# Optimization experiments

Hardware: AMD Instinct MI355X
Metric: run time of the kernel (lower is better)

## Reference

```python
import jax, jax.numpy as jnp
import numpy as np

TOPK = 80
RADIUS_GAIN = 14.0
RADIUS_MIN = 1.5
RADIUS_MAX = 18.0
EPS = 1e-6


def _norm01(x, eps=EPS):
    # per-batch min/max normalization over all non-batch dims
    b = x.shape[0]
    flat = x.reshape(b, -1)
    mn = flat.min(axis=1).reshape(b, 1, 1, 1)
    mx = flat.max(axis=1).reshape(b, 1, 1, 1)
    return (x - mn) / (mx - mn + eps)


def _avg_pool(x, k):
    # torch avg_pool2d(kernel=k, stride=1, padding=k//2, count_include_pad=True)
    s = jax.lax.reduce_window(x, 0.0, jax.lax.add, (1, 1, k, k), (1, 1, 1, 1), 'SAME')
    return s / float(k * k)


def _max_pool(x, k):
    return jax.lax.reduce_window(x, -jnp.inf, jax.lax.max, (1, 1, k, k), (1, 1, 1, 1), 'SAME')


def _compact_connected_prior(score_map):
    occ = (score_map > 0.2).astype(score_map.dtype)
    local_occ = _avg_pool(occ, 9)
    local_mass = _avg_pool(score_map, 9)
    compact = _norm01(local_occ * local_mass)
    return score_map * compact


def _gaussian_map(score_map, depth):
    b, _, h, w = score_map.shape
    dtype = score_map.dtype
    pooled = _max_pool(score_map, 5)
    maxima = score_map * (score_map == pooled).astype(dtype)  # NMS keep local maxima

    flat = maxima.reshape(b, h * w)
    vals, inds = jax.lax.top_k(flat, TOPK)              # [B,K]
    vals = jnp.where(vals > 0, vals, jnp.zeros_like(vals))  # zero-weight masked peaks

    ys = (inds // w).astype(dtype)                       # [B,K]
    xs = (inds % w).astype(dtype)
    z = jnp.take_along_axis(depth.reshape(b, h * w), inds, axis=1)
    z = jnp.maximum(z, 1e-3)
    radius = jnp.clip(RADIUS_GAIN / z, RADIUS_MIN, RADIUS_MAX)
    sigma2 = (0.6 * radius) ** 2                         # [B,K]

    yy = jnp.arange(h, dtype=dtype)
    xx = jnp.arange(w, dtype=dtype)
    dx2 = (xx[None, None, None, :] - xs[:, :, None, None]) ** 2   # [B,K,1,W]
    dy2 = (yy[None, None, :, None] - ys[:, :, None, None]) ** 2   # [B,K,H,1]
    maps = vals[:, :, None, None] * jnp.exp(
        -(dx2 + dy2) / (2.0 * sigma2[:, :, None, None] + 1e-6))    # [B,K,H,W]
    gauss = maps.max(axis=1)[:, None]                    # [B,1,H,W]; maps>=0 so zero baseline preserved
    return _norm01(gauss)


def setup_inputs() -> dict:
    key = jax.random.key(0)
    k1, k2 = jax.random.split(key)
    B, H, W = 8, 320, 320
    voxel_score_map = jax.random.uniform(k1, (B, 1, H, W), dtype=jnp.float32)
    # depth within the module's valid z range [0.3, 20.0]
    depth = 0.3 + 19.7 * jax.random.uniform(k2, (B, 1, H, W), dtype=jnp.float32)
    return {'voxel_score_map': voxel_score_map, 'depth': depth}


def reference(voxel_score_map, depth):
    compact_score = _compact_connected_prior(voxel_score_map)
    return _gaussian_map(compact_score, depth)
```

## Files before the change

kernel.cpp:

```cpp
#include <hip/hip_runtime.h>
#include <math.h>

#define HH 320
#define WW 320
#define HWP (HH * WW)
#define KTOP 80
#define CNT_STRIDE 64
#define CAP (HWP / 2)
#define TS 16
#define TPR (WW / TS)
#define TPI (TPR * (HH / TS))
#define TW 32
#define TH 64
#define NTPRX (WW / TW)
#define NTPI (NTPRX * (HH / TH))
#define LOG2E 1.4426950408889634f
#define NLOG2TAU 19.931568569324174f

__device__ __forceinline__ void wave_minmax(float& mn, float& mx) {
    for (int off = 32; off > 0; off >>= 1) {
        mn = fminf(mn, __shfl_xor(mn, off, 64));
        mx = fmaxf(mx, __shfl_xor(mx, off, 64));
    }
}

__global__ void pool_fused_k(const float* __restrict__ score, float* __restrict__ prod,
                             float2* __restrict__ pmm, int* __restrict__ cand_cnt, int B_) {
    int tid = threadIdx.x;
    if (blockIdx.x == 0)
        for (int t = tid; t < B_ * CNT_STRIDE; t += 256) cand_cnt[t] = 0;
    int blk = blockIdx.x;
    int b = blk / NTPI, t = blk % NTPI;
    int ty0 = (t / NTPRX) * TH, tx0 = (t % NTPRX) * TW;
    __shared__ float rss[TH + 8][TW + 4];
    __shared__ float rso[TH + 8][TW + 4];
    const float4* img4 = (const float4*)(score + b * HWP);
    for (int i = tid; i < (TH + 8) * (TW / 4); i += 256) {
        int r = i / (TW / 4), q = i % (TW / 4);
        int gy = ty0 - 4 + r;
        float o0=0,o1=0,o2=0,o3=0,p0=0,p1=0,p2=0,p3=0;
        if (gy >= 0 && gy < HH) {
            const float4* row4 = img4 + gy * (WW / 4);
            int gq = tx0 / 4 + q;
            float4 a = (gq > 0) ? row4[gq - 1] : make_float4(0,0,0,0);
            float4 bb = row4[gq];
            float4 c = (gq < WW / 4 - 1) ? row4[gq + 1] : make_float4(0,0,0,0);
            float w0=a.x,w1=a.y,w2=a.z,w3=a.w,w4=bb.x,w5=bb.y,w6=bb.z,w7=bb.w,w8=c.x,w9=c.y,w10=c.z,w11=c.w;
            float s = w0+w1+w2+w3+w4+w5+w6+w7+w8;
            o0=s; s+=w9-w0; o1=s; s+=w10-w1; o2=s; s+=w11-w2; o3=s;
            float c0=(w0>0.2f)?1.f:0.f, c1=(w1>0.2f)?1.f:0.f, c2=(w2>0.2f)?1.f:0.f, c3=(w3>0.2f)?1.f:0.f;
            float c4=(w4>0.2f)?1.f:0.f, c5=(w5>0.2f)?1.f:0.f, c6=(w6>0.2f)?1.f:0.f, c7=(w7>0.2f)?1.f:0.f;
            float c8=(w8>0.2f)?1.f:0.f, c9=(w9>0.2f)?1.f:0.f, c10=(w10>0.2f)?1.f:0.f, c11=(w11>0.2f)?1.f:0.f;
            float u = c0+c1+c2+c3+c4+c5+c6+c7+c8;
            p0=u; u+=c9-c0; p1=u; u+=c10-c1; p2=u; u+=c11-c2; p3=u;
        }
        *(float4*)&rss[r][q * 4] = make_float4(o0,o1,o2,o3);
        *(float4*)&rso[r][q * 4] = make_float4(p0,p1,p2,p3);
    }
    __syncthreads();
    float tmn = INFINITY, tmx = 0.f;
    const float inv81 = 1.0f / 81.0f;
    float4* pr4 = (float4*)(prod + b * HWP);
    for (int i = tid; i < TH * (TW / 4); i += 256) {
        int r = i / (TW / 4), q = i % (TW / 4);
        float sx=0,sy=0,sz=0,sw=0, ox=0,oy=0,oz=0,ow=0;
#pragma unroll
        for (int j = 0; j < 9; ++j) {
            float4 s = *(float4*)&rss[r + j][q * 4];
            float4 o = *(float4*)&rso[r + j][q * 4];
            sx+=s.x; sy+=s.y; sz+=s.z; sw+=s.w;
            ox+=o.x; oy+=o.y; oz+=o.z; ow+=o.w;
        }
        float px=(ox*inv81)*(sx*inv81), py=(oy*inv81)*(sy*inv81);
        float pz=(oz*inv81)*(sz*inv81), pw=(ow*inv81)*(sw*inv81);
        pr4[(ty0 + r) * (WW / 4) + tx0 / 4 + q] = make_float4(px,py,pz,pw);
        tmn = fminf(tmn, fminf(fminf(px,py), fminf(pz,pw)));
        tmx = fmaxf(tmx, fmaxf(fmaxf(px,py), fmaxf(pz,pw)));
    }
    wave_minmax(tmn, tmx);
    __shared__ float wmn[4], wmx[4];
    int w = tid >> 6;
    if ((tid & 63) == 0) { wmn[w] = tmn; wmx[w] = tmx; }
    __syncthreads();
    if (tid == 0)
        pmm[blk] = make_float2(fminf(fminf(wmn[0],wmn[1]), fminf(wmn[2],wmn[3])),
                               fmaxf(fmaxf(wmx[0],wmx[1]), fmaxf(wmx[2],wmx[3])));
}

__global__ void cs_nms_k(const float* __restrict__ score, const float* __restrict__ prod,
                         const float2* __restrict__ pmm, float* __restrict__ cand_base,
                         int* __restrict__ cand_cnt) {
    int tid = threadIdx.x;
    int blk = blockIdx.x;
    int b = blk / NTPI, t = blk % NTPI;
    int ty0 = (t / NTPRX) * TH, tx0 = (t % NTPRX) * TW;
    float tmn = INFINITY, tmx = 0.f;
    if (tid < NTPI) { float2 e = pmm[b * NTPI + tid]; tmn = e.x; tmx = e.y; }
    wave_minmax(tmn, tmx);
    __shared__ float s_mn, s_inv;
    if (tid == 0) { s_mn = tmn; s_inv = 1.0f / (tmx - tmn + 1e-6f); }
    __shared__ float cs[TH + 4][TW + 8 + 4];
    __shared__ float rm[TH + 4][TW + 4];
    __syncthreads();
    float mn = s_mn, inv = s_inv;
    const float4* sc4 = (const float4*)(score + b * HWP);
    const float4* pr4 = (const float4*)(prod + b * HWP);
    for (int i = tid; i < (TH + 4) * 10; i += 256) {
        int r = i / 10, q = i % 10;
        int gy = ty0 - 2 + r;
        int gq = tx0 / 4 - 1 + q;
        float4 c4 = make_float4(0,0,0,0);
        if (gy >= 0 && gy < HH && gq >= 0 && gq < WW / 4) {
            float4 s4 = sc4[gy * (WW / 4) + gq];
            float4 p4 = pr4[gy * (WW / 4) + gq];
            c4.x = s4.x * ((p4.x - mn) * inv); c4.y = s4.y * ((p4.y - mn) * inv);
            c4.z = s4.z * ((p4.z - mn) * inv); c4.w = s4.w * ((p4.w - mn) * inv);
        }
        *(float4*)&cs[r][q * 4] = c4;
    }
    __syncthreads();
    for (int i = tid; i < (TH + 4) * (TW / 4); i += 256) {
        int r = i / (TW / 4), x = (i % (TW / 4)) * 4;
        float c0=cs[r][x+2], c1=cs[r][x+3], c2=cs[r][x+4], c3=cs[r][x+5];
        float c4v=cs[r][x+6], c5=cs[r][x+7], c6=cs[r][x+8], c7=cs[r][x+9];
        float m01=fmaxf(c0,c1), m23=fmaxf(c2,c3), m45=fmaxf(c4v,c5), m67=fmaxf(c6,c7);
        float r0 = fmaxf(fmaxf(m01, m23), c4v);
        float r1 = fmaxf(fmaxf(c1, m23), m45);
        float r2 = fmaxf(fmaxf(m23, m45), c6);
        float r3 = fmaxf(fmaxf(c3, m45), m67);
        *(float4*)&rm[r][x] = make_float4(r0,r1,r2,r3);
    }
    __syncthreads();
    bool cd[8]; float vv[8]; int pb[2]; int offs[8];
#pragma unroll
    for (int qq = 0; qq < 2; ++qq) {
        int quad = qq * 256 + tid;
        int r = quad >> 3, x = (quad & 7) * 4;
        float4 v = *(float4*)&cs[r + 2][x + 4];
        float4 nm = *(float4*)&rm[r][x];
#pragma unroll
        for (int k = 1; k <= 4; ++k) {
            float4 rr = *(float4*)&rm[r + k][x];
            nm.x=fmaxf(nm.x,rr.x); nm.y=fmaxf(nm.y,rr.y);
            nm.z=fmaxf(nm.z,rr.z); nm.w=fmaxf(nm.w,rr.w);
        }
        pb[qq] = (ty0 + r) * WW + tx0 + x;
        cd[qq*4+0] = v.x > 0.f && v.x >= nm.x; vv[qq*4+0] = v.x;
        cd[qq*4+1] = v.y > 0.f && v.y >= nm.y; vv[qq*4+1] = v.y;
        cd[qq*4+2] = v.z > 0.f && v.z >= nm.z; vv[qq*4+2] = v.z;
        cd[qq*4+3] = v.w > 0.f && v.w >= nm.w; vv[qq*4+3] = v.w;
    }
    int lane = tid & 63, w = tid >> 6;
    unsigned long long lower = (1ULL << lane) - 1ULL;
    int wave_run = 0;
#pragma unroll
    for (int j = 0; j < 8; ++j) {
        unsigned long long m = __ballot(cd[j]);
        offs[j] = wave_run + __popcll(m & lower);
        wave_run += __popcll(m);
    }
    __shared__ int wbase[4];
    __shared__ int blockbase;
    if (lane == 0) wbase[w] = wave_run;
    __syncthreads();
    if (tid == 0) {
        int a0=wbase[0], a1=wbase[1], a2=wbase[2], a3=wbase[3];
        int tot = a0+a1+a2+a3;
        wbase[0]=0; wbase[1]=a0; wbase[2]=a0+a1; wbase[3]=a0+a1+a2;
        blockbase = tot ? atomicAdd(&cand_cnt[b * CNT_STRIDE], tot) : 0;
    }
    __syncthreads();
    float* cv = cand_base + b * HWP;
    int* ci = (int*)(cand_base + b * HWP + CAP);
    int bb2 = blockbase + wbase[w];
#pragma unroll
    for (int j = 0; j < 8; ++j) {
        if (cd[j]) {
            int slot = bb2 + offs[j];
            if (slot < CAP) { cv[slot] = vv[j]; ci[slot] = pb[j >> 2] + (j & 3); }
        }
    }
}

__global__ void topk_k(const float* __restrict__ cand_base, const int* __restrict__ cand_cnt,
                       const float* __restrict__ depth, float4* __restrict__ pk4g) {
    int b = blockIdx.x;
    int tid = threadIdx.x;
    int n = cand_cnt[b * CNT_STRIDE];
    if (n > CAP) n = CAP;
    const float* cv = cand_base + b * HWP;
    const int* ci = (const int*)(cand_base + b * HWP + CAP);

    __shared__ int hist[256];
    __shared__ unsigned s_prefix;
    __shared__ int s_kth;
    __shared__ float sel_v[KTOP];
    __shared__ int sel_i[KTOP];
    __shared__ int s_ng, s_nt;
    __shared__ int tie_i[512];

    if (tid == 0) { s_prefix = 0; s_kth = KTOP; s_ng = 0; s_nt = 0; }
    if (tid < KTOP) { sel_v[tid] = 0.f; sel_i[tid] = -1; }
    __syncthreads();

    if (n > KTOP) {
        for (int shift = 24; shift >= 0; shift -= 8) {
            if (tid < 256) hist[tid] = 0;
            __syncthreads();
            unsigned pref = s_prefix;
            unsigned hmask = (shift == 24) ? 0u : (0xFFFFFFFFu << (shift + 8));
            for (int i = tid; i < n; i += 1024) {
                unsigned u = __float_as_uint(cv[i]);
                if ((u & hmask) == (pref & hmask))
                    atomicAdd(&hist[(u >> shift) & 255], 1);
            }
            __syncthreads();
            if (tid < 64) {
                int h0 = hist[tid*4+0], h1 = hist[tid*4+1], h2 = hist[tid*4+2], h3 = hist[tid*4+3];
                int ls3 = h3, ls2 = h2 + ls3, ls1 = h1 + ls2, ls0 = h0 + ls1;
                int sum = ls0;
                for (int off = 1; off < 64; off <<= 1) {
                    int vv2 = __shfl_down(sum, off, 64);
                    if (tid + off < 64) sum += vv2;
                }
                int excl = sum - ls0;
                int kth = s_kth;
                int SS0=ls0+excl, SS1=ls1+excl, SS2=ls2+excl, SS3=ls3+excl, SS4=excl;
                unsigned pr = s_prefix;
                int bin = -1, rem = 0;
                if (SS0 >= kth && SS1 < kth) { bin = tid*4+0; rem = kth - SS1; }
                else if (SS1 >= kth && SS2 < kth) { bin = tid*4+1; rem = kth - SS2; }
                else if (SS2 >= kth && SS3 < kth) { bin = tid*4+2; rem = kth - SS3; }
                else if (SS3 >= kth && SS4 < kth) { bin = tid*4+3; rem = kth - SS4; }
                if (bin >= 0) { s_prefix = pr | ((unsigned)bin << shift); s_kth = rem; }
            }
            __syncthreads();
        }
        unsigned T = s_prefix;
        int need_eq = s_kth;
        for (int i = tid; i < n; i += 1024) {
            unsigned u = __float_as_uint(cv[i]);
            if (u > T) {
                int s2 = atomicAdd(&s_ng, 1);
                if (s2 < KTOP) { sel_v[s2] = cv[i]; sel_i[s2] = ci[i]; }
            } else if (u == T) {
                int s2 = atomicAdd(&s_nt, 1);
                if (s2 < 512) tie_i[s2] = ci[i];
            }
        }
        __syncthreads();
        int G = s_ng; if (G > KTOP) G = KTOP;
        int nt = s_nt; if (nt > 512) nt = 512;
        for (int t = tid; t < nt; t += 1024) {
            int mine = tie_i[t];
            int rank = 0;
            for (int j = 0; j < nt; ++j)
                if (tie_i[j] < mine) rank++;
            if (rank < need_eq && G + rank < KTOP) {
                sel_v[G + rank] = __uint_as_float(T);
                sel_i[G + rank] = mine;
            }
        }
        __syncthreads();
    } else {
        for (int i = tid; i < n; i += 1024) { sel_v[i] = cv[i]; sel_i[i] = ci[i]; }
        __syncthreads();
    }

    if (tid < KTOP) {
        float val = sel_v[tid];
        int idx = sel_i[tid];
        float xk = 0.f, yk = 0.f, wv = -1.f, lv = -INFINITY;
        if (val > 0.f && idx >= 0) {
            yk = (float)(idx / WW);
            xk = (float)(idx % WW);
            float z = fmaxf(depth[b * HWP + idx], 1e-3f);
            float r = fminf(fmaxf(14.0f / z, 1.5f), 18.0f);
            float s2 = 0.6f * r;
            s2 = s2 * s2;
            wv = -LOG2E / (2.0f * s2 + 1e-6f);
            lv = log2f(val);
        }
        pk4g[b * KTOP + tid] = make_float4(lv, xk, yk, wv);
    }
}

__global__ void gauss_tiled_k(const float4* __restrict__ pk4g, float* __restrict__ gauss,
                              float2* __restrict__ gmm) {
    int tb = blockIdx.x, tid = threadIdx.x;
    int b = tb / TPI, t = tb % TPI;
    int ty = t / TPR, tx = t % TPR;
    __shared__ float4 spk[KTOP];
    __shared__ int s_c0, s_cnt;
    bool keep = false;
    float4 pk;
    if (tid < KTOP) {
        pk = pk4g[b * KTOP + tid];
        float cut = (pk.x + NLOG2TAU) / (-pk.w);
        float x0 = (float)(tx * TS), x1 = x0 + (TS - 1);
        float y0 = (float)(ty * TS), y1 = y0 + (TS - 1);
        float cx = fminf(fmaxf(pk.y, x0), x1);
        float cy = fminf(fmaxf(pk.z, y0), y1);
        float dx = pk.y - cx, dy = pk.z - cy;
        keep = (dx * dx + dy * dy) <= cut;
    }
    int lane = tid & 63, w = tid >> 6;
    unsigned long long m = __ballot(keep);
    if (w == 0 && lane == 0) s_c0 = __popcll(m);
    __syncthreads();
    int base = (w == 0) ? 0 : s_c0;
    if (keep) spk[base + __popcll(m & ((1ULL << lane) - 1ULL))] = pk;
    if (w == 1 && lane == 0) s_cnt = s_c0 + __popcll(m);
    __syncthreads();
    int cnt = s_cnt;
    int ly = tid / TS, lx = tid % TS;
    int y = ty * TS + ly, x = tx * TS + lx;
    float fx = (float)x, fy = (float)y;
    float mval = 0.f;
    for (int i = 0; i < cnt; ++i) {
        float4 p = spk[i];
        float dx = fx - p.y, dy = fy - p.z;
        mval = fmaxf(mval, __builtin_amdgcn_exp2f(fmaf(fmaf(dx, dx, dy * dy), p.w, p.x)));
    }
    gauss[b * HWP + y * WW + x] = mval;
    float tmn = mval, tmx = mval;
    wave_minmax(tmn, tmx);
    __shared__ float wmn[4], wmx[4];
    if (lane == 0) { wmn[w] = tmn; wmx[w] = tmx; }
    __syncthreads();
    if (tid == 0)
        gmm[tb] = make_float2(fminf(fminf(wmn[0],wmn[1]), fminf(wmn[2],wmn[3])),
                              fmaxf(fmaxf(wmx[0],wmx[1]), fmaxf(wmx[2],wmx[3])));
}

__global__ void norm_k(const float* __restrict__ gauss, const float2* __restrict__ gmm,
                       float* __restrict__ out, int total) {
    int g4 = blockIdx.x * 256 + threadIdx.x;
    int b = (blockIdx.x * 1024) / HWP;
    float tmn = INFINITY, tmx = 0.f;
    {
        int t = threadIdx.x;
        if (t < TPI) { float2 e = gmm[b * TPI + t]; tmn = e.x; tmx = e.y; }
        int t2 = t + 256;
        if (t2 < TPI) { float2 e = gmm[b * TPI + t2]; tmn = fminf(tmn, e.x); tmx = fmaxf(tmx, e.y); }
    }
    wave_minmax(tmn, tmx);
    __shared__ float wmn[4], wmx[4];
    __shared__ float bmn, binv;
    int w = threadIdx.x >> 6;
    if ((threadIdx.x & 63) == 0) { wmn[w] = tmn; wmx[w] = tmx; }
    __syncthreads();
    if (threadIdx.x == 0) {
        float mn = fminf(fminf(wmn[0],wmn[1]), fminf(wmn[2],wmn[3]));
        float mx = fmaxf(fmaxf(wmx[0],wmx[1]), fmaxf(wmx[2],wmx[3]));
        bmn = mn;
        binv = 1.0f / (mx - mn + 1e-6f);
    }
    __syncthreads();
    if (g4 * 4 >= total) return;
    float4 g = ((const float4*)gauss)[g4];
    ((float4*)out)[g4] = make_float4((g.x - bmn) * binv, (g.y - bmn) * binv,
                                     (g.z - bmn) * binv, (g.w - bmn) * binv);
}

extern "C" void kernel_launch(void* const* d_in, const int* in_sizes, int n_in,
                              void* d_out, int out_size, void* d_ws, size_t ws_size,
                              hipStream_t stream) {
    const float* score = (const float*)d_in[0];
    const float* depth = (const float*)d_in[1];
    float* out = (float*)d_out;
    int total = in_sizes[0];
    int B_ = total / HWP;

    float* buf0 = (float*)d_ws;
    float* buf1 = buf0 + total;
    float* buf2 = buf1 + total;
    char* small = (char*)(buf2 + total);
    float4* pk4 = (float4*)small;
    int* cand_cnt = (int*)(small + B_ * KTOP * sizeof(float4));
    float2* pmm = (float2*)((char*)cand_cnt + B_ * CNT_STRIDE * sizeof(int));
    float2* gmm = pmm + B_ * NTPI;

    int nb4 = (total / 4 + 255) / 256;

    pool_fused_k<<<B_ * NTPI, 256, 0, stream>>>(score, buf1, pmm, cand_cnt, B_);
    cs_nms_k<<<B_ * NTPI, 256, 0, stream>>>(score, buf1, pmm, buf2, cand_cnt);
    topk_k<<<B_, 1024, 0, stream>>>(buf2, cand_cnt, depth, pk4);
    gauss_tiled_k<<<B_ * TPI, 256, 0, stream>>>(pk4, buf0, gmm);
    norm_k<<<nb4, 256, 0, stream>>>(buf0, gmm, out, total);
}
```

Before: 37.89 us.

## Fuse top-k into NMS via last-block pattern and fold normalization analytically

The top-k selection moves into the tail of the NMS kernel. A per-batch done counter picks the last finishing block, which then runs the radix select with 256 threads instead of a separate 1024-thread launch. The final min/max normalization kernel is dropped. Peak log-values are offset by log2 of the maximum peak so the gaussian output is written directly into out, assuming the map minimum is zero and the maximum equals the top peak value. This removes two launches and a full-image intermediate pass, but the serial top-k now runs on one 256-thread block per batch at the end of the NMS kernel, and it relies on that min/max assumption.

```diff
diff --git a/kernel.cpp b/kernel.cpp
--- a/kernel.cpp
+++ b/kernel.cpp
@@ -24,11 +24,14 @@
     }
 }
 
-__global__ void pool_fused_k(const float* __restrict__ score, float* __restrict__ prod,
-                             float2* __restrict__ pmm, int* __restrict__ cand_cnt, int B_) {
+__global__ __launch_bounds__(256) void pool_fused_k(
+        const float* __restrict__ score, float* __restrict__ prod,
+        float2* __restrict__ pmm, int* __restrict__ cand_cnt,
+        int* __restrict__ done_cnt, int B_) {
     int tid = threadIdx.x;
-    if (blockIdx.x == 0)
-        for (int t = tid; t < B_ * CNT_STRIDE; t += 256) cand_cnt[t] = 0;
+    if (blockIdx.x == 0) {
+        for (int t = tid; t < B_ * CNT_STRIDE; t += 256) { cand_cnt[t] = 0; done_cnt[t] = 0; }
+    }
     int blk = blockIdx.x;
     int b = blk / NTPI, t = blk % NTPI;
     int ty0 = (t / NTPRX) * TH, tx0 = (t % NTPRX) * TW;
@@ -87,9 +90,11 @@
                                fmaxf(fmaxf(wmx[0],wmx[1]), fmaxf(wmx[2],wmx[3])));
 }
 
-__global__ void cs_nms_k(const float* __restrict__ score, const float* __restrict__ prod,
-                         const float2* __restrict__ pmm, float* __restrict__ cand_base,
-                         int* __restrict__ cand_cnt) {
+__global__ __launch_bounds__(256) void cs_nms_topk_k(
+        const float* __restrict__ score, const float* __restrict__ prod,
+        const float2* __restrict__ pmm, float* __restrict__ cand_base,
+        int* __restrict__ cand_cnt, int* __restrict__ done_cnt,
+        const float* __restrict__ depth, float4* __restrict__ pk4g) {
     int tid = threadIdx.x;
     int blk = blockIdx.x;
     int b = blk / NTPI, t = blk % NTPI;
@@ -170,23 +175,23 @@
         blockbase = tot ? atomicAdd(&cand_cnt[b * CNT_STRIDE], tot) : 0;
     }
     __syncthreads();
-    float* cv = cand_base + b * HWP;
-    int* ci = (int*)(cand_base + b * HWP + CAP);
+    float* cv_w = cand_base + b * HWP;
+    int* ci_w = (int*)(cand_base + b * HWP + CAP);
     int bb2 = blockbase + wbase[w];
 #pragma unroll
     for (int j = 0; j < 8; ++j) {
         if (cd[j]) {
             int slot = bb2 + offs[j];
-            if (slot < CAP) { cv[slot] = vv[j]; ci[slot] = pb[j >> 2] + (j & 3); }
-        }
-    }
-}
-
-__global__ void topk_k(const float* __restrict__ cand_base, const int* __restrict__ cand_cnt,
-                       const float* __restrict__ depth, float4* __restrict__ pk4g) {
-    int b = blockIdx.x;
-    int tid = threadIdx.x;
-    int n = cand_cnt[b * CNT_STRIDE];
+            if (slot < CAP) { cv_w[slot] = vv[j]; ci_w[slot] = pb[j >> 2] + (j & 3); }
+        }
+    }
+    __threadfence();
+    __shared__ int s_last;
+    if (tid == 0) s_last = atomicAdd(&done_cnt[b * CNT_STRIDE], 1);
+    __syncthreads();
+    if (s_last != NTPI - 1) return;
+    __threadfence();
+    int n = atomicAdd(&cand_cnt[b * CNT_STRIDE], 0);
     if (n > CAP) n = CAP;
     const float* cv = cand_base + b * HWP;
     const int* ci = (const int*)(cand_base + b * HWP + CAP);
@@ -205,11 +210,11 @@
 
     if (n > KTOP) {
         for (int shift = 24; shift >= 0; shift -= 8) {
-            if (tid < 256) hist[tid] = 0;
+            hist[tid] = 0;
             __syncthreads();
             unsigned pref = s_prefix;
             unsigned hmask = (shift == 24) ? 0u : (0xFFFFFFFFu << (shift + 8));
-            for (int i = tid; i < n; i += 1024) {
+            for (int i = tid; i < n; i += 256) {
                 unsigned u = __float_as_uint(cv[i]);
                 if ((u & hmask) == (pref & hmask))
                     atomicAdd(&hist[(u >> shift) & 255], 1);
@@ -238,7 +243,7 @@
         }
         unsigned T = s_prefix;
         int need_eq = s_kth;
-        for (int i = tid; i < n; i += 1024) {
+        for (int i = tid; i < n; i += 256) {
             unsigned u = __float_as_uint(cv[i]);
             if (u > T) {
                 int s2 = atomicAdd(&s_ng, 1);
@@ -251,8 +256,8 @@
         __syncthreads();
         int G = s_ng; if (G > KTOP) G = KTOP;
         int nt = s_nt; if (nt > 512) nt = 512;
-        for (int t = tid; t < nt; t += 1024) {
-            int mine = tie_i[t];
+        for (int t2 = tid; t2 < nt; t2 += 256) {
+            int mine = tie_i[t2];
             int rank = 0;
             for (int j = 0; j < nt; ++j)
                 if (tie_i[j] < mine) rank++;
@@ -263,9 +268,17 @@
         }
         __syncthreads();
     } else {
-        for (int i = tid; i < n; i += 1024) { sel_v[i] = cv[i]; sel_i[i] = ci[i]; }
+        for (int i = tid; i < n; i += 256) { sel_v[i] = cv[i]; sel_i[i] = ci[i]; }
         __syncthreads();
     }
+
+    float vmv = (tid < KTOP) ? sel_v[tid] : 0.f;
+    for (int off = 32; off > 0; off >>= 1) vmv = fmaxf(vmv, __shfl_xor(vmv, off, 64));
+    __shared__ float wvx[4];
+    if (lane == 0) wvx[w] = vmv;
+    __syncthreads();
+    float vmax = fmaxf(fmaxf(wvx[0], wvx[1]), fmaxf(wvx[2], wvx[3]));
+    float lvoff = log2f(vmax + 1e-6f);
 
     if (tid < KTOP) {
         float val = sel_v[tid];
@@ -279,14 +292,14 @@
             float s2 = 0.6f * r;
             s2 = s2 * s2;
             wv = -LOG2E / (2.0f * s2 + 1e-6f);
-            lv = log2f(val);
+            lv = log2f(val) - lvoff;
         }
         pk4g[b * KTOP + tid] = make_float4(lv, xk, yk, wv);
     }
 }
 
-__global__ void gauss_tiled_k(const float4* __restrict__ pk4g, float* __restrict__ gauss,
-                              float2* __restrict__ gmm) {
+__global__ __launch_bounds__(256) void gauss_out_k(const float4* __restrict__ pk4g,
+                                                   float* __restrict__ out) {
     int tb = blockIdx.x, tid = threadIdx.x;
     int b = tb / TPI, t = tb % TPI;
     int ty = t / TPR, tx = t % TPR;
@@ -322,45 +335,7 @@
         float dx = fx - p.y, dy = fy - p.z;
         mval = fmaxf(mval, __builtin_amdgcn_exp2f(fmaf(fmaf(dx, dx, dy * dy), p.w, p.x)));
     }
-    gauss[b * HWP + y * WW + x] = mval;
-    float tmn = mval, tmx = mval;
-    wave_minmax(tmn, tmx);
-    __shared__ float wmn[4], wmx[4];
-    if (lane == 0) { wmn[w] = tmn; wmx[w] = tmx; }
-    __syncthreads();
-    if (tid == 0)
-        gmm[tb] = make_float2(fminf(fminf(wmn[0],wmn[1]), fminf(wmn[2],wmn[3])),
-                              fmaxf(fmaxf(wmx[0],wmx[1]), fmaxf(wmx[2],wmx[3])));
-}
-
-__global__ void norm_k(const float* __restrict__ gauss, const float2* __restrict__ gmm,
-                       float* __restrict__ out, int total) {
-    int g4 = blockIdx.x * 256 + threadIdx.x;
-    int b = (blockIdx.x * 1024) / HWP;
-    float tmn = INFINITY, tmx = 0.f;
-    {
-        int t = threadIdx.x;
-        if (t < TPI) { float2 e = gmm[b * TPI + t]; tmn = e.x; tmx = e.y; }
-        int t2 = t + 256;
-        if (t2 < TPI) { float2 e = gmm[b * TPI + t2]; tmn = fminf(tmn, e.x); tmx = fmaxf(tmx, e.y); }
-    }
-    wave_minmax(tmn, tmx);
-    __shared__ float wmn[4], wmx[4];
-    __shared__ float bmn, binv;
-    int w = threadIdx.x >> 6;
-    if ((threadIdx.x & 63) == 0) { wmn[w] = tmn; wmx[w] = tmx; }
-    __syncthreads();
-    if (threadIdx.x == 0) {
-        float mn = fminf(fminf(wmn[0],wmn[1]), fminf(wmn[2],wmn[3]));
-        float mx = fmaxf(fmaxf(wmx[0],wmx[1]), fmaxf(wmx[2],wmx[3]));
-        bmn = mn;
-        binv = 1.0f / (mx - mn + 1e-6f);
-    }
-    __syncthreads();
-    if (g4 * 4 >= total) return;
-    float4 g = ((const float4*)gauss)[g4];
-    ((float4*)out)[g4] = make_float4((g.x - bmn) * binv, (g.y - bmn) * binv,
-                                     (g.z - bmn) * binv, (g.w - bmn) * binv);
+    out[b * HWP + y * WW + x] = mval;
 }
 
 extern "C" void kernel_launch(void* const* d_in, const int* in_sizes, int n_in,
@@ -372,20 +347,16 @@
     int total = in_sizes[0];
     int B_ = total / HWP;
 
-    float* buf0 = (float*)d_ws;
-    float* buf1 = buf0 + total;
+    float* buf1 = (float*)d_ws;
     float* buf2 = buf1 + total;
     char* small = (char*)(buf2 + total);
     float4* pk4 = (float4*)small;
     int* cand_cnt = (int*)(small + B_ * KTOP * sizeof(float4));
-    float2* pmm = (float2*)((char*)cand_cnt + B_ * CNT_STRIDE * sizeof(int));
-    float2* gmm = pmm + B_ * NTPI;
-
-    int nb4 = (total / 4 + 255) / 256;
-
-    pool_fused_k<<<B_ * NTPI, 256, 0, stream>>>(score, buf1, pmm, cand_cnt, B_);
-    cs_nms_k<<<B_ * NTPI, 256, 0, stream>>>(score, buf1, pmm, buf2, cand_cnt);
-    topk_k<<<B_, 1024, 0, stream>>>(buf2, cand_cnt, depth, pk4);
-    gauss_tiled_k<<<B_ * TPI, 256, 0, stream>>>(pk4, buf0, gmm);
-    norm_k<<<nb4, 256, 0, stream>>>(buf0, gmm, out, total);
-}
+    int* done_cnt = cand_cnt + B_ * CNT_STRIDE;
+    float2* pmm = (float2*)(done_cnt + B_ * CNT_STRIDE);
+
+    pool_fused_k<<<B_ * NTPI, 256, 0, stream>>>(score, buf1, pmm, cand_cnt, done_cnt, B_);
+    cs_nms_topk_k<<<B_ * NTPI, 256, 0, stream>>>(score, buf1, pmm, buf2, cand_cnt,
+                                                 done_cnt, depth, pk4);
+    gauss_out_k<<<B_ * TPI, 256, 0, stream>>>(pk4, out);
+}
```

After: 78.35 us. +106.8%, slower.
